# Performance work log

Measured on AMD Instinct MI355X. Metric: run time of the kernel, lower is better.

## Reference

```python
import jax, jax.numpy as jnp
import numpy as np

N_HEADS = 12
D_MODEL = 768
D_HEAD = 64
LN_EPS = 1e-5


def setup_inputs() -> dict:
    key = jax.random.key(0)
    ks = jax.random.split(key, 7)
    bs, slen = 1, 4096
    s_in = 1.0 / np.sqrt(D_MODEL)
    s_out = 1.0 / np.sqrt(N_HEADS * D_HEAD)
    return {
        "x": jax.random.normal(ks[0], (bs, slen, D_MODEL), jnp.float32),
        "W_attn": jax.random.uniform(ks[1], (D_MODEL, 3 * N_HEADS * D_HEAD), jnp.float32, -s_in, s_in),
        "b_attn": jax.random.uniform(ks[2], (3 * N_HEADS * D_HEAD,), jnp.float32, -s_in, s_in),
        "W_out": jax.random.uniform(ks[3], (N_HEADS * D_HEAD, D_MODEL), jnp.float32, -s_out, s_out),
        "b_out": jax.random.uniform(ks[4], (D_MODEL,), jnp.float32, -s_out, s_out),
        "ln_g": jnp.ones((D_MODEL,), jnp.float32),
        "ln_b": jnp.zeros((D_MODEL,), jnp.float32),
    }


def reference(x, W_attn, b_attn, W_out, b_out, ln_g, ln_b):
    bs, slen, _ = x.shape
    qkv = x @ W_attn + b_attn                      # [b, s, 3*H*D]
    wq, wk, wv = jnp.split(qkv, 3, axis=-1)
    def to_heads(t):
        return t.reshape(bs, slen, N_HEADS, D_HEAD)
    q, k, v = to_heads(wq), to_heads(wk), to_heads(wv)
    # scores: [b, h, s_q, s_k]
    scores = jnp.einsum('bqhd,bkhd->bhqk', q, k) / np.sqrt(D_HEAD).astype(np.float32)
    probs = jax.nn.softmax(scores, axis=-1)
    attn = jnp.einsum('bhqk,bkhd->bqhd', probs, v).reshape(bs, slen, N_HEADS * D_HEAD)
    out = attn @ W_out + b_out
    y = x + out
    mu = jnp.mean(y, axis=-1, keepdims=True)
    var = jnp.mean(jnp.square(y - mu), axis=-1, keepdims=True)
    return (y - mu) / jnp.sqrt(var + LN_EPS) * ln_g + ln_b
```

## Files before the change

kernel.cpp:

```cpp
#include <hip/hip_runtime.h>
#include <cstdint>
#include <cstddef>

#define SL 4096
#define DM 768

typedef short s16x8 __attribute__((ext_vector_type(8)));
typedef unsigned short u16x8 __attribute__((ext_vector_type(8)));
typedef unsigned short u16x4 __attribute__((ext_vector_type(4)));
typedef float f32x4 __attribute__((ext_vector_type(4)));
typedef float f32x16 __attribute__((ext_vector_type(16)));
typedef unsigned int u32x4 __attribute__((ext_vector_type(4)));

__device__ __forceinline__ unsigned short f2bf(float f) {
  unsigned u = __float_as_uint(f);
  u = u + 0x7fffu + ((u >> 16) & 1u);
  return (unsigned short)(u >> 16);
}

__device__ __forceinline__ int swz(int row, int col) {
  return (row << 6) + ((((col >> 3) ^ row) & 7) << 3) + (col & 7);
}

__device__ __forceinline__ int aswz(int row, int col) {
  return (row << 6) + ((((col >> 3) ^ row ^ (row >> 3)) & 7) << 3) + (col & 7);
}

__device__ __forceinline__ int vswz(int d, int col) {
  return (d << 5) + ((((col >> 3) ^ (d >> 1)) & 3) << 3) + (col & 7);
}

#define ASYNC16(G, L)                                                        \
  __builtin_amdgcn_global_load_lds(                                          \
      (const __attribute__((address_space(1))) void*)(G),                    \
      (__attribute__((address_space(3))) void*)(L), 16, 0, 0)

#define WAITB()                                   \
  do {                                            \
    asm volatile("s_waitcnt vmcnt(0)" ::: "memory"); \
    __builtin_amdgcn_s_barrier();                 \
  } while (0)

extern "C" __global__ __launch_bounds__(256) void k_cvt(
    const float* __restrict__ in, unsigned short* __restrict__ out, int n) {
  int i = (blockIdx.x * 256 + threadIdx.x) * 4;
  if (i >= n) return;
  f32x4 v = *reinterpret_cast<const f32x4*>(in + i);
  u16x4 o;
  o[0] = f2bf(v[0]); o[1] = f2bf(v[1]); o[2] = f2bf(v[2]); o[3] = f2bf(v[3]);
  *reinterpret_cast<u16x4*>(out + i) = o;
}

extern "C" __global__ __launch_bounds__(256) void k_tr(
    const float* __restrict__ in, unsigned short* __restrict__ out, int R, int C) {
  __shared__ float tile[64][65];
  const int t = threadIdx.x;
  const int r0 = blockIdx.y * 64, c0 = blockIdx.x * 64;
  const int lr = t >> 2, lcb = (t & 3) * 16;
  #pragma unroll
  for (int j = 0; j < 16; j += 4) {
    f32x4 v = *reinterpret_cast<const f32x4*>(in + (size_t)(r0 + lr) * C + c0 + lcb + j);
    tile[lr][lcb + j + 0] = v[0];
    tile[lr][lcb + j + 1] = v[1];
    tile[lr][lcb + j + 2] = v[2];
    tile[lr][lcb + j + 3] = v[3];
  }
  __syncthreads();
  #pragma unroll
  for (int j = 0; j < 16; j += 4) {
    u16x4 o;
    o[0] = f2bf(tile[lcb + j + 0][lr]);
    o[1] = f2bf(tile[lcb + j + 1][lr]);
    o[2] = f2bf(tile[lcb + j + 2][lr]);
    o[3] = f2bf(tile[lcb + j + 3][lr]);
    *reinterpret_cast<u16x4*>(out + (size_t)(c0 + lr) * R + r0 + lcb + j) = o;
  }
}

__device__ __forceinline__ void gemm_body(
    const unsigned short* al, const unsigned short* bl, f32x4* acc,
    int wv, int l15, int lg) {
  #pragma unroll
  for (int kc = 0; kc < 2; kc++) {
    s16x8 af = *reinterpret_cast<const s16x8*>(&al[swz(wv * 16 + l15, kc * 32 + lg * 8)]);
    #pragma unroll
    for (int nt = 0; nt < 4; nt++) {
      s16x8 bfr = *reinterpret_cast<const s16x8*>(&bl[swz(nt * 16 + l15, kc * 32 + lg * 8)]);
      acc[nt] = __builtin_amdgcn_mfma_f32_16x16x32_bf16(af, bfr, acc[nt], 0, 0, 0);
    }
  }
}

extern "C" __global__ __launch_bounds__(256) void k_qkv(
    const unsigned short* __restrict__ xbf, const unsigned short* __restrict__ wt,
    const float* __restrict__ bias, unsigned short* __restrict__ qb,
    unsigned short* __restrict__ kbo, unsigned short* __restrict__ vt) {
  __shared__ alignas(16) unsigned short a_lds[2][4096];
  __shared__ alignas(16) unsigned short b_lds[2][4096];
  const int t = threadIdx.x, wv = t >> 6, l = t & 63;
  const int l15 = l & 15, lg = l >> 4;
  const int m0 = blockIdx.y * 64, n0 = blockIdx.x * 64;
  f32x4 acc[4];
  acc[0] = acc[1] = acc[2] = acc[3] = (f32x4)0.f;
  int soff[2];
  #pragma unroll
  for (int c = 0; c < 2; c++) {
    int idx = wv * 128 + c * 64 + l;
    int row = idx >> 3, bp = idx & 7;
    int cb = (bp ^ row) & 7;
    soff[c] = row * DM + cb * 8;
  }
  const unsigned short* asrc = xbf + (size_t)m0 * DM;
  const unsigned short* bsrc = wt + (size_t)n0 * DM;
  unsigned short* la = &a_lds[0][0];
  unsigned short* lb = &b_lds[0][0];

#define STAGE_AB(B, KK)                                              \
  do {                                                               \
    ASYNC16(asrc + (KK) + soff[0], la + (B)*4096 + wv * 1024);       \
    ASYNC16(asrc + (KK) + soff[1], la + (B)*4096 + wv * 1024 + 512); \
    ASYNC16(bsrc + (KK) + soff[0], lb + (B)*4096 + wv * 1024);       \
    ASYNC16(bsrc + (KK) + soff[1], lb + (B)*4096 + wv * 1024 + 512); \
  } while (0)

  STAGE_AB(0, 0);
  WAITB();
  for (int kk = 0; kk < DM; kk += 128) {
    STAGE_AB(1, kk + 64);
    gemm_body(&a_lds[0][0], &b_lds[0][0], acc, wv, l15, lg);
    WAITB();
    if (kk + 128 < DM) STAGE_AB(0, kk + 128);
    gemm_body(&a_lds[1][0], &b_lds[1][0], acc, wv, l15, lg);
    WAITB();
  }
#undef STAGE_AB
  const int mb = m0 + wv * 16 + lg * 4;
  #pragma unroll
  for (int nt = 0; nt < 4; nt++) {
    const int n = n0 + nt * 16 + l15;
    const float bv = bias[n];
    const int sec = n / DM;
    const int nn = n - sec * DM;
    const int h = nn >> 6, d = nn & 63;
    if (sec == 0) {
      #pragma unroll
      for (int r = 0; r < 4; r++)
        qb[((size_t)h * SL + mb + r) * 64 + d] = f2bf((acc[nt][r] + bv) * 0.180336880f);
    } else if (sec == 1) {
      #pragma unroll
      for (int r = 0; r < 4; r++)
        kbo[((size_t)h * SL + mb + r) * 64 + d] = f2bf(acc[nt][r] + bv);
    } else {
      u16x4 o;
      #pragma unroll
      for (int r = 0; r < 4; r++) o[r] = f2bf(acc[nt][r] + bv);
      *reinterpret_cast<u16x4*>(vt + ((size_t)h * 64 + d) * SL + mb) = o;
    }
  }
}

__device__ __forceinline__ void attn_body32s(
    const unsigned short* kb, const unsigned short* vb,
    const s16x8* qf, f32x16* ot, float& mrun, float& lrun,
    int l31, int s) {
  f32x16 st = (f32x16)0.f;
  __builtin_amdgcn_s_setprio(1);
  #pragma unroll
  for (int c = 0; c < 4; c++) {
    s16x8 kf = *reinterpret_cast<const s16x8*>(&kb[aswz(l31, c * 16 + s * 8)]);
    st = __builtin_amdgcn_mfma_f32_32x32x16_bf16(kf, qf[c], st, 0, 0, 0);
  }
  __builtin_amdgcn_s_setprio(0);
  float m8[8];
  #pragma unroll
  for (int i = 0; i < 8; i++) m8[i] = fmaxf(st[i], st[i + 8]);
  float m4a = fmaxf(m8[0], m8[4]), m4b = fmaxf(m8[1], m8[5]);
  float m4c = fmaxf(m8[2], m8[6]), m4d = fmaxf(m8[3], m8[7]);
  float tm = fmaxf(fmaxf(m4a, m4b), fmaxf(m4c, m4d));
  float xa = tm, xb = tm;
  asm volatile("v_permlane32_swap_b32 %0, %1" : "+v"(xa), "+v"(xb));
  const float rowmax = fmaxf(xa, xb);
  if (!__all(rowmax <= mrun + 10.0f)) {
    const float mn = fmaxf(mrun, rowmax);
    const float corr = exp2f(mrun - mn);
    lrun *= corr;
    #pragma unroll
    for (int dt = 0; dt < 2; dt++)
      #pragma unroll
      for (int r = 0; r < 16; r++) ot[dt][r] *= corr;
    mrun = mn;
  }
  float p0 = 0.f, p1 = 0.f, p2 = 0.f, p3 = 0.f;
  #pragma unroll
  for (int r = 0; r < 16; r += 4) {
    float e0 = exp2f(st[r + 0] - mrun);
    float e1 = exp2f(st[r + 1] - mrun);
    float e2 = exp2f(st[r + 2] - mrun);
    float e3 = exp2f(st[r + 3] - mrun);
    st[r + 0] = e0; st[r + 1] = e1; st[r + 2] = e2; st[r + 3] = e3;
    p0 += e0; p1 += e1; p2 += e2; p3 += e3;
  }
  float psum = (p0 + p1) + (p2 + p3);
  float sa = psum, sb = psum;
  asm volatile("v_permlane32_swap_b32 %0, %1" : "+v"(sa), "+v"(sb));
  lrun += sa + sb;
  __builtin_amdgcn_s_setprio(1);
  #pragma unroll
  for (int m = 0; m < 2; m++) {
    const int m0 = m * 8;
    unsigned w0, w1, w2, w3;
    asm("v_cvt_pk_bf16_f32 %0, %1, %2" : "=v"(w0) : "v"(st[m0 + 0]), "v"(st[m0 + 1]));
    asm("v_cvt_pk_bf16_f32 %0, %1, %2" : "=v"(w1) : "v"(st[m0 + 2]), "v"(st[m0 + 3]));
    asm("v_cvt_pk_bf16_f32 %0, %1, %2" : "=v"(w2) : "v"(st[m0 + 4]), "v"(st[m0 + 5]));
    asm("v_cvt_pk_bf16_f32 %0, %1, %2" : "=v"(w3) : "v"(st[m0 + 6]), "v"(st[m0 + 7]));
    asm volatile("v_permlane32_swap_b32 %0, %1" : "+v"(w0), "+v"(w2));
    asm volatile("v_permlane32_swap_b32 %0, %1" : "+v"(w1), "+v"(w3));
    u32x4 wv_;
    wv_[0] = w0; wv_[1] = w1; wv_[2] = w2; wv_[3] = w3;
    s16x8 pbf = *reinterpret_cast<s16x8*>(&wv_);
    #pragma unroll
    for (int dt = 0; dt < 2; dt++) {
      s16x8 vf = *reinterpret_cast<const s16x8*>(&vb[vswz(dt * 32 + l31, m * 16 + s * 8)]);
      ot[dt] = __builtin_amdgcn_mfma_f32_32x32x16_bf16(vf, pbf, ot[dt], 0, 0, 0);
    }
  }
  __builtin_amdgcn_s_setprio(0);
}

extern "C" __global__ __launch_bounds__(256) void k_attn(
    const unsigned short* __restrict__ qb, const unsigned short* __restrict__ kbi,
    const unsigned short* __restrict__ vt, unsigned short* __restrict__ aout) {
  __shared__ alignas(16) unsigned short k_lds[2][2][2048];
  __shared__ alignas(16) unsigned short v_lds[2][2][2048];
  __shared__ float o_mrg[2][32][68];
  __shared__ float ml_mrg[2][32][2];
  const int t = threadIdx.x, w = t >> 6, l = t & 63;
  const int l31 = l & 31, s = l >> 5;
  const int half = w >> 1, qs = w & 1;
  const int bid = blockIdx.x;
  const int sid = (bid & 7) * 96 + (bid >> 3);
  const int h = sid >> 6, qt = sid & 63;
  const unsigned short* qh = qb + (size_t)h * SL * 64;
  const unsigned short* kh = kbi + (size_t)h * SL * 64 + (size_t)half * 2048 * 64;
  const unsigned short* vh = vt + (size_t)h * 64 * SL + half * 2048;
  const int q = qt * 64 + qs * 32 + l31;
  s16x8 qf[4];
  #pragma unroll
  for (int c = 0; c < 4; c++)
    qf[c] = *reinterpret_cast<const s16x8*>(qh + (size_t)q * 64 + c * 16 + s * 8);
  f32x16 ot[2];
  ot[0] = (f32x16)0.f;
  ot[1] = (f32x16)0.f;
  float mrun = -1e30f, lrun = 0.f;
  int koff[2], voff[2];
  #pragma unroll
  for (int c = 0; c < 2; c++) {
    int i = (qs * 2 + c) * 64 + l;
    int key = i >> 3, kb_ = i & 7;
    koff[c] = key * 64 + (kb_ ^ ((key ^ (key >> 3)) & 7)) * 8;
    int d = i >> 2, vb_ = i & 3;
    voff[c] = d * SL + (vb_ ^ ((d >> 1) & 3)) * 8;
  }

#define STAGE_KV(B, LB)                                                     \
  do {                                                                      \
    _Pragma("unroll")                                                       \
    for (int c = 0; c < 2; c++) {                                           \
      ASYNC16(kh + (size_t)(LB) * 64 + koff[c],                             \
              &k_lds[half][B][0] + (qs * 2 + c) * 512);                     \
      ASYNC16(vh + (LB) + voff[c],                                          \
              &v_lds[half][B][0] + (qs * 2 + c) * 512);                     \
    }                                                                       \
  } while (0)

  STAGE_KV(0, 0);
  WAITB();
  for (int lb = 0; lb < 2048; lb += 64) {
    STAGE_KV(1, lb + 32);
    attn_body32s(&k_lds[half][0][0], &v_lds[half][0][0], qf, ot, mrun, lrun, l31, s);
    WAITB();
    if (lb + 64 < 2048) STAGE_KV(0, lb + 64);
    attn_body32s(&k_lds[half][1][0], &v_lds[half][1][0], qf, ot, mrun, lrun, l31, s);
    WAITB();
  }
#undef STAGE_KV
  if (half == 1) {
    #pragma unroll
    for (int dt = 0; dt < 2; dt++) {
      #pragma unroll
      for (int rq = 0; rq < 4; rq++) {
        f32x4 v;
        #pragma unroll
        for (int j = 0; j < 4; j++) v[j] = ot[dt][rq * 4 + j];
        *reinterpret_cast<f32x4*>(&o_mrg[qs][l31][dt * 32 + rq * 8 + s * 4]) = v;
      }
    }
    if (s == 0) {
      ml_mrg[qs][l31][0] = mrun;
      ml_mrg[qs][l31][1] = lrun;
    }
  }
  __syncthreads();
  if (half == 0) {
    const float mB = ml_mrg[qs][l31][0], lB = ml_mrg[qs][l31][1];
    const float mn = fmaxf(mrun, mB);
    const float cA = exp2f(mrun - mn), cB = exp2f(mB - mn);
    const float linv = 1.f / (lrun * cA + lB * cB);
    #pragma unroll
    for (int dt = 0; dt < 2; dt++) {
      #pragma unroll
      for (int rq = 0; rq < 4; rq++) {
        f32x4 vb_ = *reinterpret_cast<const f32x4*>(&o_mrg[qs][l31][dt * 32 + rq * 8 + s * 4]);
        u16x4 o;
        #pragma unroll
        for (int j = 0; j < 4; j++)
          o[j] = f2bf((ot[dt][rq * 4 + j] * cA + vb_[j] * cB) * linv);
        *reinterpret_cast<u16x4*>(aout + (size_t)q * DM + h * 64 + dt * 32 + rq * 8 + s * 4) = o;
      }
    }
  }
}

extern "C" __global__ __launch_bounds__(256) void k_out(
    const unsigned short* __restrict__ abf, const unsigned short* __restrict__ wot,
    const float* __restrict__ bias, const float* __restrict__ x, float* __restrict__ y) {
  __shared__ alignas(16) unsigned short a_lds[2][4096];
  __shared__ alignas(16) unsigned short b_lds[2][4096];
  const int t = threadIdx.x, wv = t >> 6, l = t & 63;
  const int l15 = l & 15, lg = l >> 4;
  const int m0 = blockIdx.y * 64, n0 = blockIdx.x * 64;
  f32x4 acc[4];
  acc[0] = acc[1] = acc[2] = acc[3] = (f32x4)0.f;
  int soff[2];
  #pragma unroll
  for (int c = 0; c < 2; c++) {
    int idx = wv * 128 + c * 64 + l;
    int row = idx >> 3, bp = idx & 7;
    int cb = (bp ^ row) & 7;
    soff[c] = row * DM + cb * 8;
  }
  const unsigned short* asrc = abf + (size_t)m0 * DM;
  const unsigned short* bsrc = wot + (size_t)n0 * DM;
  unsigned short* la = &a_lds[0][0];
  unsigned short* lb = &b_lds[0][0];

#define STAGE_AB(B, KK)                                              \
  do {                                                               \
    ASYNC16(asrc + (KK) + soff[0], la + (B)*4096 + wv * 1024);       \
    ASYNC16(asrc + (KK) + soff[1], la + (B)*4096 + wv * 1024 + 512); \
    ASYNC16(bsrc + (KK) + soff[0], lb + (B)*4096 + wv * 1024);       \
    ASYNC16(bsrc + (KK) + soff[1], lb + (B)*4096 + wv * 1024 + 512); \
  } while (0)

  STAGE_AB(0, 0);
  WAITB();
  for (int kk = 0; kk < DM; kk += 128) {
    STAGE_AB(1, kk + 64);
    gemm_body(&a_lds[0][0], &b_lds[0][0], acc, wv, l15, lg);
    WAITB();
    if (kk + 128 < DM) STAGE_AB(0, kk + 128);
    gemm_body(&a_lds[1][0], &b_lds[1][0], acc, wv, l15, lg);
    WAITB();
  }
#undef STAGE_AB
  const int mb = m0 + wv * 16 + lg * 4;
  #pragma unroll
  for (int nt = 0; nt < 4; nt++) {
    const int n = n0 + nt * 16 + l15;
    const float bv = bias[n];
    #pragma unroll
    for (int r = 0; r < 4; r++)
      y[(size_t)(mb + r) * DM + n] = acc[nt][r] + bv + x[(size_t)(mb + r) * DM + n];
  }
}

extern "C" __global__ __launch_bounds__(256) void k_ln(
    const float* __restrict__ y, const float* __restrict__ g, const float* __restrict__ b,
    float* __restrict__ out) {
  const int row = blockIdx.x, t = threadIdx.x;
  const float* yr = y + (size_t)row * DM;
  float v0 = yr[t], v1 = yr[t + 256], v2 = yr[t + 512];
  float sum = v0 + v1 + v2;
  float sq = v0 * v0 + v1 * v1 + v2 * v2;
  #pragma unroll
  for (int off = 1; off < 64; off <<= 1) {
    sum += __shfl_xor(sum, off, 64);
    sq += __shfl_xor(sq, off, 64);
  }
  __shared__ float ls[8];
  const int wv = t >> 6, l = t & 63;
  if (l == 0) { ls[wv] = sum; ls[4 + wv] = sq; }
  __syncthreads();
  sum = ls[0] + ls[1] + ls[2] + ls[3];
  sq = ls[4] + ls[5] + ls[6] + ls[7];
  const float mu = sum * (1.f / DM);
  const float rstd = rsqrtf(sq * (1.f / DM) - mu * mu + 1e-5f);
  out[(size_t)row * DM + t] = (v0 - mu) * rstd * g[t] + b[t];
  out[(size_t)row * DM + t + 256] = (v1 - mu) * rstd * g[t + 256] + b[t + 256];
  out[(size_t)row * DM + t + 512] = (v2 - mu) * rstd * g[t + 512] + b[t + 512];
}

extern "C" void kernel_launch(void* const* d_in, const int* in_sizes, int n_in,
                              void* d_out, int out_size, void* d_ws, size_t ws_size,
                              hipStream_t stream) {
  (void)in_sizes; (void)n_in; (void)out_size; (void)ws_size;
  const float* x = (const float*)d_in[0];
  const float* Wa = (const float*)d_in[1];
  const float* ba = (const float*)d_in[2];
  const float* Wo = (const float*)d_in[3];
  const float* bo = (const float*)d_in[4];
  const float* lng = (const float*)d_in[5];
  const float* lnb = (const float*)d_in[6];
  float* out = (float*)d_out;

  unsigned short* ws16 = (unsigned short*)d_ws;
  unsigned short* xbf = ws16;
  unsigned short* wat = xbf + 3145728;
  unsigned short* wot = wat + 1769472;
  unsigned short* qbf = wot + 589824;
  unsigned short* kbf = qbf + 3145728;
  unsigned short* vtb = kbf + 3145728;
  unsigned short* aob = vtb + 3145728;
  float* ybuf = (float*)(aob + 3145728);

  k_cvt<<<3072, 256, 0, stream>>>(x, xbf, 3145728);
  k_tr<<<dim3(36, 12), 256, 0, stream>>>(Wa, wat, 768, 2304);
  k_tr<<<dim3(12, 12), 256, 0, stream>>>(Wo, wot, 768, 768);
  k_qkv<<<dim3(36, 64), 256, 0, stream>>>(xbf, wat, ba, qbf, kbf, vtb);
  k_attn<<<768, 256, 0, stream>>>(qbf, kbf, vtb, aob);
  k_out<<<dim3(12, 64), 256, 0, stream>>>(aob, wot, bo, x, ybuf);
  k_ln<<<4096, 256, 0, stream>>>(ybuf, lng, lnb, out);
}
```

Measured before the change: 179.3 us.

## Replace online softmax max tracking with precomputed Cauchy-Schwarz score bound

Two small kernels are added. One computes the per-head maximum key norm and the other computes a per-query bound M = |q|·max|k|. The attention kernel then subtracts this fixed bound instead of keeping a running max, which removes the row-max reduction, the permlane swaps and the conditional output rescaling. Row sums are now accumulated with an extra MFMA against a ones vector, and the final merge of the two key halves becomes a plain add. The cost is two extra launches plus a memset, and a risk of exp underflow or lost precision when the bound is far above the true maximum score.

```diff
diff --git a/kernel.cpp b/kernel.cpp
--- a/kernel.cpp
+++ b/kernel.cpp
@@ -159,52 +159,63 @@
   }
 }
 
-__device__ __forceinline__ void attn_body32s(
+extern "C" __global__ __launch_bounds__(256) void k_kmax(
+    const unsigned short* __restrict__ kbf, unsigned* __restrict__ kmax) {
+  const int h = blockIdx.x >> 4, part = blockIdx.x & 15;
+  const unsigned short* row = kbf + ((size_t)h * SL + part * 256 + threadIdx.x) * 64;
+  float ss = 0.f;
+  #pragma unroll
+  for (int j = 0; j < 64; j += 8) {
+    u16x8 v = *reinterpret_cast<const u16x8*>(row + j);
+    #pragma unroll
+    for (int e = 0; e < 8; e++) {
+      float f = __uint_as_float((unsigned)v[e] << 16);
+      ss = fmaf(f, f, ss);
+    }
+  }
+  #pragma unroll
+  for (int off = 1; off < 64; off <<= 1) ss = fmaxf(ss, __shfl_xor(ss, off, 64));
+  __shared__ float red[4];
+  if ((threadIdx.x & 63) == 0) red[threadIdx.x >> 6] = ss;
+  __syncthreads();
+  if (threadIdx.x == 0) {
+    float m = fmaxf(fmaxf(red[0], red[1]), fmaxf(red[2], red[3]));
+    atomicMax(kmax + h, __float_as_uint(sqrtf(m)));
+  }
+}
+
+extern "C" __global__ __launch_bounds__(256) void k_qbnd(
+    const unsigned short* __restrict__ qbf, const unsigned* __restrict__ kmax,
+    float* __restrict__ M) {
+  const int idx = blockIdx.x * 256 + threadIdx.x;
+  const unsigned short* row = qbf + (size_t)idx * 64;
+  float ss = 0.f;
+  #pragma unroll
+  for (int j = 0; j < 64; j += 8) {
+    u16x8 v = *reinterpret_cast<const u16x8*>(row + j);
+    #pragma unroll
+    for (int e = 0; e < 8; e++) {
+      float f = __uint_as_float((unsigned)v[e] << 16);
+      ss = fmaf(f, f, ss);
+    }
+  }
+  M[idx] = sqrtf(ss) * __uint_as_float(kmax[idx >> 12]);
+}
+
+__device__ __forceinline__ void attn_body32f(
     const unsigned short* kb, const unsigned short* vb,
-    const s16x8* qf, f32x16* ot, float& mrun, float& lrun,
-    int l31, int s) {
+    const s16x8* qf, f32x16* ot, f32x16& lacc, float negM,
+    const int* kfo, const int* vfo, s16x8 ones) {
   f32x16 st = (f32x16)0.f;
   __builtin_amdgcn_s_setprio(1);
   #pragma unroll
   for (int c = 0; c < 4; c++) {
-    s16x8 kf = *reinterpret_cast<const s16x8*>(&kb[aswz(l31, c * 16 + s * 8)]);
+    s16x8 kf = *reinterpret_cast<const s16x8*>(&kb[kfo[c]]);
     st = __builtin_amdgcn_mfma_f32_32x32x16_bf16(kf, qf[c], st, 0, 0, 0);
   }
   __builtin_amdgcn_s_setprio(0);
-  float m8[8];
-  #pragma unroll
-  for (int i = 0; i < 8; i++) m8[i] = fmaxf(st[i], st[i + 8]);
-  float m4a = fmaxf(m8[0], m8[4]), m4b = fmaxf(m8[1], m8[5]);
-  float m4c = fmaxf(m8[2], m8[6]), m4d = fmaxf(m8[3], m8[7]);
-  float tm = fmaxf(fmaxf(m4a, m4b), fmaxf(m4c, m4d));
-  float xa = tm, xb = tm;
-  asm volatile("v_permlane32_swap_b32 %0, %1" : "+v"(xa), "+v"(xb));
-  const float rowmax = fmaxf(xa, xb);
-  if (!__all(rowmax <= mrun + 10.0f)) {
-    const float mn = fmaxf(mrun, rowmax);
-    const float corr = exp2f(mrun - mn);
-    lrun *= corr;
-    #pragma unroll
-    for (int dt = 0; dt < 2; dt++)
-      #pragma unroll
-      for (int r = 0; r < 16; r++) ot[dt][r] *= corr;
-    mrun = mn;
-  }
-  float p0 = 0.f, p1 = 0.f, p2 = 0.f, p3 = 0.f;
-  #pragma unroll
-  for (int r = 0; r < 16; r += 4) {
-    float e0 = exp2f(st[r + 0] - mrun);
-    float e1 = exp2f(st[r + 1] - mrun);
-    float e2 = exp2f(st[r + 2] - mrun);
-    float e3 = exp2f(st[r + 3] - mrun);
-    st[r + 0] = e0; st[r + 1] = e1; st[r + 2] = e2; st[r + 3] = e3;
-    p0 += e0; p1 += e1; p2 += e2; p3 += e3;
-  }
-  float psum = (p0 + p1) + (p2 + p3);
-  float sa = psum, sb = psum;
-  asm volatile("v_permlane32_swap_b32 %0, %1" : "+v"(sa), "+v"(sb));
-  lrun += sa + sb;
-  __builtin_amdgcn_s_setprio(1);
+  #pragma unroll
+  for (int r = 0; r < 16; r++) st[r] = exp2f(st[r] + negM);
   #pragma unroll
   for (int m = 0; m < 2; m++) {
     const int m0 = m * 8;
@@ -218,22 +229,24 @@
     u32x4 wv_;
     wv_[0] = w0; wv_[1] = w1; wv_[2] = w2; wv_[3] = w3;
     s16x8 pbf = *reinterpret_cast<s16x8*>(&wv_);
+    __builtin_amdgcn_s_setprio(1);
     #pragma unroll
     for (int dt = 0; dt < 2; dt++) {
-      s16x8 vf = *reinterpret_cast<const s16x8*>(&vb[vswz(dt * 32 + l31, m * 16 + s * 8)]);
+      s16x8 vf = *reinterpret_cast<const s16x8*>(&vb[vfo[m * 2 + dt]]);
       ot[dt] = __builtin_amdgcn_mfma_f32_32x32x16_bf16(vf, pbf, ot[dt], 0, 0, 0);
     }
-  }
-  __builtin_amdgcn_s_setprio(0);
+    lacc = __builtin_amdgcn_mfma_f32_32x32x16_bf16(ones, pbf, lacc, 0, 0, 0);
+    __builtin_amdgcn_s_setprio(0);
+  }
 }
 
 extern "C" __global__ __launch_bounds__(256) void k_attn(
     const unsigned short* __restrict__ qb, const unsigned short* __restrict__ kbi,
-    const unsigned short* __restrict__ vt, unsigned short* __restrict__ aout) {
-  __shared__ alignas(16) unsigned short k_lds[2][2][2048];
-  __shared__ alignas(16) unsigned short v_lds[2][2][2048];
-  __shared__ float o_mrg[2][32][68];
-  __shared__ float ml_mrg[2][32][2];
+    const unsigned short* __restrict__ vt, const float* __restrict__ Mb,
+    unsigned short* __restrict__ aout) {
+  __shared__ alignas(16) unsigned char smem[32768];
+  unsigned short* kst = (unsigned short*)smem;
+  unsigned short* vst = (unsigned short*)(smem + 16384);
   const int t = threadIdx.x, w = t >> 6, l = t & 63;
   const int l31 = l & 31, s = l >> 5;
   const int half = w >> 1, qs = w & 1;
@@ -244,14 +257,18 @@
   const unsigned short* kh = kbi + (size_t)h * SL * 64 + (size_t)half * 2048 * 64;
   const unsigned short* vh = vt + (size_t)h * 64 * SL + half * 2048;
   const int q = qt * 64 + qs * 32 + l31;
+  const float negM = -Mb[h * SL + q];
   s16x8 qf[4];
   #pragma unroll
   for (int c = 0; c < 4; c++)
     qf[c] = *reinterpret_cast<const s16x8*>(qh + (size_t)q * 64 + c * 16 + s * 8);
+  s16x8 ones;
+  #pragma unroll
+  for (int e = 0; e < 8; e++) ones[e] = (short)0x3F80;
   f32x16 ot[2];
   ot[0] = (f32x16)0.f;
   ot[1] = (f32x16)0.f;
-  float mrun = -1e30f, lrun = 0.f;
+  f32x16 lacc = (f32x16)0.f;
   int koff[2], voff[2];
   #pragma unroll
   for (int c = 0; c < 2; c++) {
@@ -261,15 +278,22 @@
     int d = i >> 2, vb_ = i & 3;
     voff[c] = d * SL + (vb_ ^ ((d >> 1) & 3)) * 8;
   }
+  int kfo[4], vfo[4];
+  #pragma unroll
+  for (int c = 0; c < 4; c++) kfo[c] = aswz(l31, c * 16 + s * 8);
+  #pragma unroll
+  for (int m = 0; m < 2; m++)
+    #pragma unroll
+    for (int dt = 0; dt < 2; dt++) vfo[m * 2 + dt] = vswz(dt * 32 + l31, m * 16 + s * 8);
 
 #define STAGE_KV(B, LB)                                                     \
   do {                                                                      \
     _Pragma("unroll")                                                       \
     for (int c = 0; c < 2; c++) {                                           \
       ASYNC16(kh + (size_t)(LB) * 64 + koff[c],                             \
-              &k_lds[half][B][0] + (qs * 2 + c) * 512);                     \
+              kst + (half * 2 + (B)) * 2048 + (qs * 2 + c) * 512);          \
       ASYNC16(vh + (LB) + voff[c],                                          \
-              &v_lds[half][B][0] + (qs * 2 + c) * 512);                     \
+              vst + (half * 2 + (B)) * 2048 + (qs * 2 + c) * 512);          \
     }                                                                       \
   } while (0)
 
@@ -277,13 +301,19 @@
   WAITB();
   for (int lb = 0; lb < 2048; lb += 64) {
     STAGE_KV(1, lb + 32);
-    attn_body32s(&k_lds[half][0][0], &v_lds[half][0][0], qf, ot, mrun, lrun, l31, s);
+    attn_body32f(kst + (half * 2) * 2048, vst + (half * 2) * 2048,
+                 qf, ot, lacc, negM, kfo, vfo, ones);
     WAITB();
     if (lb + 64 < 2048) STAGE_KV(0, lb + 64);
-    attn_body32s(&k_lds[half][1][0], &v_lds[half][1][0], qf, ot, mrun, lrun, l31, s);
+    attn_body32f(kst + (half * 2 + 1) * 2048, vst + (half * 2 + 1) * 2048,
+                 qf, ot, lacc, negM, kfo, vfo, ones);
     WAITB();
   }
 #undef STAGE_KV
+  const float lsum = lacc[0];
+  float* o_m = (float*)smem;
+  float* l_m = (float*)(smem + 17408);
+  __syncthreads();
   if (half == 1) {
     #pragma unroll
     for (int dt = 0; dt < 2; dt++) {
@@ -292,29 +322,23 @@
         f32x4 v;
         #pragma unroll
         for (int j = 0; j < 4; j++) v[j] = ot[dt][rq * 4 + j];
-        *reinterpret_cast<f32x4*>(&o_mrg[qs][l31][dt * 32 + rq * 8 + s * 4]) = v;
+        *reinterpret_cast<f32x4*>(&o_m[(qs * 32 + l31) * 68 + dt * 32 + rq * 8 + s * 4]) = v;
       }
     }
-    if (s == 0) {
-      ml_mrg[qs][l31][0] = mrun;
-      ml_mrg[qs][l31][1] = lrun;
-    }
+    if (s == 0) l_m[qs * 32 + l31] = lsum;
   }
   __syncthreads();
   if (half == 0) {
-    const float mB = ml_mrg[qs][l31][0], lB = ml_mrg[qs][l31][1];
-    const float mn = fmaxf(mrun, mB);
-    const float cA = exp2f(mrun - mn), cB = exp2f(mB - mn);
-    const float linv = 1.f / (lrun * cA + lB * cB);
+    const float linv = 1.f / (lsum + l_m[qs * 32 + l31]);
     #pragma unroll
     for (int dt = 0; dt < 2; dt++) {
       #pragma unroll
       for (int rq = 0; rq < 4; rq++) {
-        f32x4 vb_ = *reinterpret_cast<const f32x4*>(&o_mrg[qs][l31][dt * 32 + rq * 8 + s * 4]);
+        f32x4 vb_ = *reinterpret_cast<const f32x4*>(&o_m[(qs * 32 + l31) * 68 + dt * 32 + rq * 8 + s * 4]);
         u16x4 o;
         #pragma unroll
         for (int j = 0; j < 4; j++)
-          o[j] = f2bf((ot[dt][rq * 4 + j] * cA + vb_[j] * cB) * linv);
+          o[j] = f2bf((ot[dt][rq * 4 + j] + vb_[j]) * linv);
         *reinterpret_cast<u16x4*>(aout + (size_t)q * DM + h * 64 + dt * 32 + rq * 8 + s * 4) = o;
       }
     }
@@ -422,12 +446,17 @@
   unsigned short* vtb = kbf + 3145728;
   unsigned short* aob = vtb + 3145728;
   float* ybuf = (float*)(aob + 3145728);
-
+  float* Mb = ybuf + 3145728;
+  unsigned* kmx = (unsigned*)(Mb + 49152);
+
+  hipMemsetAsync(kmx, 0, 12 * sizeof(unsigned), stream);
   k_cvt<<<3072, 256, 0, stream>>>(x, xbf, 3145728);
   k_tr<<<dim3(36, 12), 256, 0, stream>>>(Wa, wat, 768, 2304);
   k_tr<<<dim3(12, 12), 256, 0, stream>>>(Wo, wot, 768, 768);
   k_qkv<<<dim3(36, 64), 256, 0, stream>>>(xbf, wat, ba, qbf, kbf, vtb);
-  k_attn<<<768, 256, 0, stream>>>(qbf, kbf, vtb, aob);
+  k_kmax<<<192, 256, 0, stream>>>(kbf, kmx);
+  k_qbnd<<<192, 256, 0, stream>>>(qbf, kmx, Mb);
+  k_attn<<<768, 256, 0, stream>>>(qbf, kbf, vtb, Mb, aob);
   k_out<<<dim3(12, 64), 256, 0, stream>>>(aob, wot, bo, x, ybuf);
   k_ln<<<4096, 256, 0, stream>>>(ybuf, lng, lnb, out);
 }
```

Result: no change. 180.6 us (+0.7%).
